# Kernel optimization log

Hardware: AMD Instinct MI355X
Metric: run time of the kernel (lower is better)

Reference implementation:

```python
import jax, jax.numpy as jnp
import numpy as np

N, F, E, C = 50000, 128, 800000, 10

def setup_inputs() -> dict:
    key = jax.random.key(0)
    ks = jax.random.split(key, 16)
    s = 1.0 / np.sqrt(F)
    def u(k, shape):
        return jax.random.uniform(k, shape, jnp.float32, -s, s)
    inp = {
        "x": jax.random.normal(ks[0], (N, F), jnp.float32),
        "edge_index": jax.random.randint(ks[1], (2, E), 0, N),
    }
    for i, p in enumerate(["1", "2"]):
        b = 2 + i * 5
        inp["W" + p] = u(ks[b], (F, F))          # EvolveGCNO initial_weight
        inp["wih" + p] = u(ks[b + 1], (3 * F, F))  # GRU input weights (r,z,n)
        inp["whh" + p] = u(ks[b + 2], (3 * F, F))  # GRU hidden weights
        inp["bih" + p] = u(ks[b + 3], (3 * F,))
        inp["bhh" + p] = u(ks[b + 4], (3 * F,))
    inp["lin_w"] = u(ks[12], (C, F))
    inp["lin_b"] = u(ks[13], (C,))
    return inp

def gru_step(x, h, wih, whh, bih, bhh):
    # torch.nn.GRU single step; gate order r, z, n
    gi = x @ wih.T + bih
    gh = h @ whh.T + bhh
    ir, iz, inn = jnp.split(gi, 3, axis=-1)
    hr, hz, hn = jnp.split(gh, 3, axis=-1)
    r = jax.nn.sigmoid(ir + hr)
    z = jax.nn.sigmoid(iz + hz)
    n = jnp.tanh(inn + r * hn)
    return (1.0 - z) * n + z * h

def gcn_conv(W, x, src, dst):
    # GCNConv_Fixed_W: gcn_norm with self-loops, then aggregate (x @ W)
    n = x.shape[0]
    loop = jnp.arange(n)
    s = jnp.concatenate([src, loop])
    d = jnp.concatenate([dst, loop])
    deg = jax.ops.segment_sum(jnp.ones(s.shape[0], x.dtype), d, num_segments=n)
    dinv = jnp.where(deg > 0, jax.lax.rsqrt(deg), 0.0)
    norm = dinv[s] * dinv[d]                 # [E+N]
    xw = x @ W                               # [N, F]
    return jax.ops.segment_sum(norm[:, None] * xw[s], d, num_segments=n)

def evolve_gcno(x, src, dst, W0, wih, whh, bih, bhh):
    # weight evolved by GRU with input = hidden = current weight
    W = gru_step(W0, W0, wih, whh, bih, bhh)
    return gcn_conv(W, x, src, dst)

def reference(x, edge_index, W1, wih1, whh1, bih1, bhh1,
              W2, wih2, whh2, bih2, bhh2, lin_w, lin_b):
    src, dst = edge_index[0], edge_index[1]
    h = jax.nn.relu(evolve_gcno(x, src, dst, W1, wih1, whh1, bih1, bhh1))
    # dropout is identity in eval mode
    h = jax.nn.relu(evolve_gcno(h, src, dst, W2, wih2, whh2, bih2, bhh2))
    logits = h @ lin_w.T + lin_b
    return jax.nn.log_softmax(logits, axis=1)
```

## Files before the change

kernel.cpp:

```cpp
#include <hip/hip_runtime.h>
#include <cstddef>
#include <cstdint>

#define F 128
#define C_OUT 10
#define SB 256
#define SLOTS 128

typedef short bf16x8 __attribute__((ext_vector_type(8)));
typedef float f32x4  __attribute__((ext_vector_type(4)));
typedef float f32x2  __attribute__((ext_vector_type(2)));

__device__ __forceinline__ unsigned short bf16_rne(float f) {
  unsigned u = __float_as_uint(f);
  return (unsigned short)((u + 0x7FFFu + ((u >> 16) & 1u)) >> 16);
}

__device__ __forceinline__ void gather8(
    const char* p0, const char* p1, const char* p2, const char* p3,
    const char* p4, const char* p5, const char* p6, const char* p7,
    unsigned& u0, unsigned& u1, unsigned& u2, unsigned& u3,
    unsigned& u4, unsigned& u5, unsigned& u6, unsigned& u7) {
  asm volatile(
      "global_load_dword %0, %[q0], off\n\t"
      "global_load_dword %1, %[q1], off\n\t"
      "global_load_dword %2, %[q2], off\n\t"
      "global_load_dword %3, %[q3], off\n\t"
      "global_load_dword %4, %[q4], off\n\t"
      "global_load_dword %5, %[q5], off\n\t"
      "global_load_dword %6, %[q6], off\n\t"
      "global_load_dword %7, %[q7], off\n\t"
      "s_waitcnt vmcnt(0)"
      : "=&v"(u0), "=&v"(u1), "=&v"(u2), "=&v"(u3),
        "=&v"(u4), "=&v"(u5), "=&v"(u6), "=&v"(u7)
      : [q0] "v"(p0), [q1] "v"(p1), [q2] "v"(p2), [q3] "v"(p3),
        [q4] "v"(p4), [q5] "v"(p5), [q6] "v"(p6), [q7] "v"(p7));
}

__device__ __forceinline__ void gather4(
    const char* p0, const char* p1, const char* p2, const char* p3,
    unsigned& u0, unsigned& u1, unsigned& u2, unsigned& u3) {
  asm volatile(
      "global_load_dword %0, %[q0], off\n\t"
      "global_load_dword %1, %[q1], off\n\t"
      "global_load_dword %2, %[q2], off\n\t"
      "global_load_dword %3, %[q3], off\n\t"
      "s_waitcnt vmcnt(0)"
      : "=&v"(u0), "=&v"(u1), "=&v"(u2), "=&v"(u3)
      : [q0] "v"(p0), [q1] "v"(p1), [q2] "v"(p2), [q3] "v"(p3));
}

__global__ void gru_evolve2_k(const float* __restrict__ W01, const float* __restrict__ wih1,
                              const float* __restrict__ whh1, const float* __restrict__ bih1,
                              const float* __restrict__ bhh1,
                              const float* __restrict__ W02, const float* __restrict__ wih2,
                              const float* __restrict__ whh2, const float* __restrict__ bih2,
                              const float* __restrict__ bhh2,
                              unsigned short* __restrict__ Bhi1, unsigned short* __restrict__ Bhi2,
                              int* __restrict__ counts, int n) {
  if ((int)blockIdx.x >= 128) {
    int i = ((int)blockIdx.x - 128) * SB + threadIdx.x;
    if (i < n) counts[i] = 0;
    return;
  }
  int t = blockIdx.x * 256 + threadIdx.x;
  int layer = t >> 14;
  int tt = t & 16383;
  const float* W0  = layer ? W02  : W01;
  const float* wih = layer ? wih2 : wih1;
  const float* whh = layer ? whh2 : whh1;
  const float* bih = layer ? bih2 : bih1;
  const float* bhh = layer ? bhh2 : bhh1;
  unsigned short* Bhi = layer ? Bhi2 : Bhi1;
  int i = tt >> 7, j = tt & 127;
  const float4* w0r = (const float4*)(W0 + (size_t)i * F);
  float gi[3], gh[3];
#pragma unroll
  for (int g = 0; g < 3; ++g) {
    const float4* wr = (const float4*)(wih + (size_t)(g * F + j) * F);
    const float4* hr = (const float4*)(whh + (size_t)(g * F + j) * F);
    float si = 0.f, sh = 0.f;
    for (int k = 0; k < F / 4; ++k) {
      float4 a = w0r[k];
      float4 b = wr[k];
      float4 c = hr[k];
      si += a.x * b.x + a.y * b.y + a.z * b.z + a.w * b.w;
      sh += a.x * c.x + a.y * c.y + a.z * c.z + a.w * c.w;
    }
    gi[g] = si + bih[g * F + j];
    gh[g] = sh + bhh[g * F + j];
  }
  float r = 1.0f / (1.0f + expf(-(gi[0] + gh[0])));
  float z = 1.0f / (1.0f + expf(-(gi[1] + gh[1])));
  float nn = tanhf(gi[2] + r * gh[2]);
  float val = (1.0f - z) * nn + z * W0[(size_t)i * F + j];

  int kstep = i >> 5, kl = i & 31;
  int lane = (kl >> 3) * 16 + (j & 15);
  int tile = j >> 4;
  int idx = ((kstep * 8 + tile) * 64 + lane) * 8 + (kl & 7);
  Bhi[idx] = bf16_rne(val);
}

__global__ void count_rank_k(const int* __restrict__ dst, int* __restrict__ counts,
                             int* __restrict__ rank, int E) {
  int e = blockIdx.x * blockDim.x + threadIdx.x;
  if (e < E) rank[e] = atomicAdd(&counts[dst[e]], 1);
}

__device__ __forceinline__ void fill_body(int bid, const int* __restrict__ src,
                                          const int* __restrict__ dst,
                                          const int* __restrict__ rank,
                                          int* __restrict__ csr_slot, int E) {
  int e = bid * 256 + (int)threadIdx.x;
  if (e < E) {
    int r = rank[e];
    if (r < SLOTS)
      csr_slot[((size_t)dst[e] << 7) + r] = src[e] << 7;
  }
}

__device__ __forceinline__ void gemm_body(int bid, const float* __restrict__ X,
                                          const unsigned short* __restrict__ Bhi,
                                          const int* __restrict__ counts,
                                          unsigned* __restrict__ Y, int nrows) {
  int wid = bid * 4 + ((int)threadIdx.x >> 6);
  int lane = threadIdx.x & 63;
  int ng = (nrows + 15) >> 4;
  if (wid >= ng) return;
  int g = __builtin_amdgcn_readfirstlane(wid);
  int q = lane >> 4, m = lane & 15;
  int rowA = g * 16 + m;
  if (rowA >= nrows) rowA = nrows - 1;

  f32x4 acc[8];
#pragma unroll
  for (int t = 0; t < 8; ++t) { acc[t].x = 0.f; acc[t].y = 0.f; acc[t].z = 0.f; acc[t].w = 0.f; }

#pragma unroll
  for (int s = 0; s < 4; ++s) {
    const float* xp = X + (size_t)rowA * F + s * 32 + q * 8;
    float4 xa = *(const float4*)xp;
    float4 xb = *(const float4*)(xp + 4);
    float xv[8] = {xa.x, xa.y, xa.z, xa.w, xb.x, xb.y, xb.z, xb.w};
    bf16x8 xh;
#pragma unroll
    for (int j = 0; j < 8; ++j) xh[j] = (short)bf16_rne(xv[j]);
#pragma unroll
    for (int t = 0; t < 8; ++t) {
      size_t boff = ((size_t)(s * 8 + t) * 64 + lane) * 8;
      bf16x8 wh = *(const bf16x8*)(Bhi + boff);
      acc[t] = __builtin_amdgcn_mfma_f32_16x16x32_bf16(wh, xh, acc[t], 0, 0, 0);
    }
  }

  int row = g * 16 + m;
  if (row < nrows) {
    float dd = rsqrtf((float)counts[row] + 1.0f);
    unsigned* yr = Y + (size_t)row * 32 + q;
#pragma unroll
    for (int t = 0; t < 8; ++t) {
      int p = __builtin_amdgcn_cvt_pk_fp8_f32(dd * acc[t].x, dd * acc[t].y, 0, false);
      p = __builtin_amdgcn_cvt_pk_fp8_f32(dd * acc[t].z, dd * acc[t].w, p, true);
      yr[t * 4] = (unsigned)p;
    }
  }
}

__global__ void gemm_mfma_k(const float* __restrict__ X, const unsigned short* __restrict__ Bhi,
                            const int* __restrict__ counts, unsigned* __restrict__ Y,
                            int nrows) {
  gemm_body(blockIdx.x, X, Bhi, counts, Y, nrows);
}

__global__ void fill_gemm_k(const float* __restrict__ X, const unsigned short* __restrict__ Bhi,
                            const int* __restrict__ counts, unsigned* __restrict__ Y,
                            int nrows, int ngemm,
                            const int* __restrict__ src, const int* __restrict__ dst,
                            const int* __restrict__ rank, int* __restrict__ csr_slot, int E) {
  if ((int)blockIdx.x < ngemm)
    gemm_body(blockIdx.x, X, Bhi, counts, Y, nrows);
  else
    fill_body((int)blockIdx.x - ngemm, src, dst, rank, csr_slot, E);
}

template <bool FUSE_LOGITS>
__global__ void agg_fp8_k(const int* __restrict__ counts, const int* __restrict__ csr_slot,
                          const unsigned* __restrict__ xwp,
                          float* __restrict__ hout,
                          const float* __restrict__ lw, const float* __restrict__ lb,
                          float* __restrict__ outp, int n) {
  int wave = (int)((blockIdx.x * blockDim.x + threadIdx.x) >> 6);
  int lane = threadIdx.x & 63;
  if (wave >= n) return;
  int node = __builtin_amdgcn_readfirstlane(wave);
  int half = lane >> 5, hm = lane & 31;
  const char* __restrict__ cb = (const char*)xwp;
  unsigned loff = (unsigned)(hm << 2);
  const int* __restrict__ row = csr_slot + ((size_t)node << 7);

  int e = counts[node];
  float dd = rsqrtf((float)e + 1.0f);
  f32x2 acc0 = {0.f, 0.f}, acc1 = {0.f, 0.f};
  f32x2 bcc0 = {0.f, 0.f}, bcc1 = {0.f, 0.f};

#define DEC(U, A, B)                                           \
  do {                                                         \
    (A) += __builtin_amdgcn_cvt_pk_f32_fp8((int)(U), false);   \
    (B) += __builtin_amdgcn_cvt_pk_f32_fp8((int)(U), true);    \
  } while (0)

  {
    unsigned u = *(const unsigned*)(cb + ((((unsigned)node) << 7) | loff));
    if (half) u = 0u;
    DEC(u, acc0, acc1);
  }

  const int* __restrict__ cp = row + half;
  int i = 0;
  for (; i + 16 <= e; i += 16) {
    int s0 = cp[i + 0],  s1 = cp[i + 2],  s2 = cp[i + 4],  s3 = cp[i + 6];
    int s4 = cp[i + 8],  s5 = cp[i + 10], s6 = cp[i + 12], s7 = cp[i + 14];
    unsigned u0, u1, u2, u3, u4, u5, u6, u7;
    gather8(cb + (((unsigned)s0) | loff), cb + (((unsigned)s1) | loff),
            cb + (((unsigned)s2) | loff), cb + (((unsigned)s3) | loff),
            cb + (((unsigned)s4) | loff), cb + (((unsigned)s5) | loff),
            cb + (((unsigned)s6) | loff), cb + (((unsigned)s7) | loff),
            u0, u1, u2, u3, u4, u5, u6, u7);
    DEC(u0, acc0, acc1);
    DEC(u1, bcc0, bcc1);
    DEC(u2, acc0, acc1);
    DEC(u3, bcc0, bcc1);
    DEC(u4, acc0, acc1);
    DEC(u5, bcc0, bcc1);
    DEC(u6, acc0, acc1);
    DEC(u7, bcc0, bcc1);
  }
  if (i + 8 <= e) {
    int s0 = cp[i + 0], s1 = cp[i + 2], s2 = cp[i + 4], s3 = cp[i + 6];
    unsigned u0, u1, u2, u3;
    gather4(cb + (((unsigned)s0) | loff), cb + (((unsigned)s1) | loff),
            cb + (((unsigned)s2) | loff), cb + (((unsigned)s3) | loff),
            u0, u1, u2, u3);
    DEC(u0, acc0, acc1);
    DEC(u1, bcc0, bcc1);
    DEC(u2, acc0, acc1);
    DEC(u3, bcc0, bcc1);
    i += 8;
  }
  if (i + 4 <= e) {
    int s0 = cp[i + 0], s1 = cp[i + 2];
    unsigned u0 = *(const unsigned*)(cb + (((unsigned)s0) | loff));
    unsigned u1 = *(const unsigned*)(cb + (((unsigned)s1) | loff));
    DEC(u0, acc0, acc1);
    DEC(u1, bcc0, bcc1);
    i += 4;
  }
  if (i + 2 <= e) {
    int s0 = cp[i];
    unsigned u = *(const unsigned*)(cb + (((unsigned)s0) | loff));
    DEC(u, acc0, acc1);
    i += 2;
  }
  if (i < e) {
    int idx = i + half;
    if (idx >= e) idx = e - 1;
    int s = row[idx];
    unsigned u = *(const unsigned*)(cb + (((unsigned)s) | loff));
    if (half) u = 0u;
    DEC(u, bcc0, bcc1);
  }
#undef DEC
  acc0 += bcc0;
  acc1 += bcc1;

  acc0.x += __shfl_xor(acc0.x, 32);
  acc0.y += __shfl_xor(acc0.y, 32);
  acc1.x += __shfl_xor(acc1.x, 32);
  acc1.y += __shfl_xor(acc1.y, 32);

  float h0 = fmaxf(dd * acc0.x, 0.f);
  float h1 = fmaxf(dd * acc0.y, 0.f);
  float h2 = fmaxf(dd * acc1.x, 0.f);
  float h3 = fmaxf(dd * acc1.y, 0.f);

  if (!FUSE_LOGITS) {
    if (half == 0) {
      *(float4*)(hout + (size_t)node * F + hm * 4) = make_float4(h0, h1, h2, h3);
    }
  } else {
    float acc[C_OUT];
#pragma unroll
    for (int c = 0; c < C_OUT; ++c) {
      float4 w = *(const float4*)(lw + (size_t)c * F + hm * 4);
      float v = h0 * w.x + h1 * w.y + h2 * w.z + h3 * w.w;
      v += __shfl_xor(v, 1); v += __shfl_xor(v, 2);
      v += __shfl_xor(v, 4); v += __shfl_xor(v, 8);
      v += __shfl_xor(v, 16);
      acc[c] = v + lb[c];
    }
    float mx = acc[0];
#pragma unroll
    for (int c = 1; c < C_OUT; ++c) mx = fmaxf(mx, acc[c]);
    float s = 0.f;
#pragma unroll
    for (int c = 0; c < C_OUT; ++c) s += expf(acc[c] - mx);
    float lse = mx + logf(s);
#pragma unroll
    for (int c = 0; c < C_OUT; ++c)
      if (lane == c) outp[(size_t)node * C_OUT + c] = acc[c] - lse;
  }
}

extern "C" void kernel_launch(void* const* d_in, const int* in_sizes, int n_in,
                              void* d_out, int out_size, void* d_ws, size_t ws_size,
                              hipStream_t stream) {
  const float* x    = (const float*)d_in[0];
  const int*   ei   = (const int*)d_in[1];
  const float* W1   = (const float*)d_in[2];
  const float* wih1 = (const float*)d_in[3];
  const float* whh1 = (const float*)d_in[4];
  const float* bih1 = (const float*)d_in[5];
  const float* bhh1 = (const float*)d_in[6];
  const float* W2   = (const float*)d_in[7];
  const float* wih2 = (const float*)d_in[8];
  const float* whh2 = (const float*)d_in[9];
  const float* bih2 = (const float*)d_in[10];
  const float* bhh2 = (const float*)d_in[11];
  const float* lw   = (const float*)d_in[12];
  const float* lb   = (const float*)d_in[13];
  float* out = (float*)d_out;

  int N = in_sizes[0] / F;
  int E = in_sizes[1] / 2;
  const int* src = ei;
  const int* dst = ei + E;
  int nb = (N + SB - 1) / SB;
  int ng = (N + 15) / 16;
  int ngemm = (ng + 3) / 4;
  int nfill = (E + 255) / 256;
  int nagg = (N + 3) / 4;

  float* ws = (float*)d_ws;
  unsigned* bufA = (unsigned*)ws;
  float* bufB = (float*)(bufA + (size_t)N * 32);
  unsigned short* Bhi1 = (unsigned short*)(bufB + (size_t)N * F);
  unsigned short* Bhi2 = Bhi1 + F * F;
  int* counts = (int*)(Bhi2 + F * F);
  int* rank   = counts + N;
  int* csr_slot = rank + E;

  gru_evolve2_k<<<128 + nb, 256, 0, stream>>>(W1, wih1, whh1, bih1, bhh1,
                                              W2, wih2, whh2, bih2, bhh2,
                                              Bhi1, Bhi2, counts, N);
  count_rank_k<<<(E + 255) / 256, 256, 0, stream>>>(dst, counts, rank, E);
  fill_gemm_k<<<ngemm + nfill, 256, 0, stream>>>(x, Bhi1, counts, bufA, N, ngemm,
                                                 src, dst, rank, csr_slot, E);
  agg_fp8_k<false><<<nagg, 256, 0, stream>>>(counts, csr_slot, bufA, bufB,
                                             nullptr, nullptr, nullptr, N);
  gemm_mfma_k<<<ngemm, 256, 0, stream>>>(bufB, Bhi2, counts, bufA, N);
  agg_fp8_k<true><<<nagg, 256, 0, stream>>>(counts, csr_slot, bufA, nullptr,
                                            lw, lb, out, N);
}
```

Baseline: 258.4 us.

## Fuse all stages into one persistent kernel with grid barriers

Replaces the six-kernel pipeline with a single persistent kernel of 1024 blocks that runs GRU evolution, edge counting and CSR fill, both GEMMs and both aggregations, separated by software grid barriers. The count and fill passes are merged so the rank array is no longer stored, and the layer-1 GEMM main loop runs before the edge pass so its accumulators stay in registers across a barrier. This is meant to remove kernel launch gaps and the rank round-trip through memory. In exchange it depends on all 1024 blocks being co-resident, and it fixes occupancy with launch bounds, uses grid-stride loops for aggregation and adds a memset for the barrier counter.

```diff
diff --git a/kernel.cpp b/kernel.cpp
--- a/kernel.cpp
+++ b/kernel.cpp
@@ -4,8 +4,10 @@
 
 #define F 128
 #define C_OUT 10
-#define SB 256
 #define SLOTS 128
+#define GRID_BLOCKS 1024
+#define NTHR (GRID_BLOCKS * 256)
+#define NWAVES (NTHR / 64)
 
 typedef short bf16x8 __attribute__((ext_vector_type(8)));
 typedef float f32x4  __attribute__((ext_vector_type(4)));
@@ -50,20 +52,26 @@
       : [q0] "v"(p0), [q1] "v"(p1), [q2] "v"(p2), [q3] "v"(p3));
 }
 
-__global__ void gru_evolve2_k(const float* __restrict__ W01, const float* __restrict__ wih1,
-                              const float* __restrict__ whh1, const float* __restrict__ bih1,
-                              const float* __restrict__ bhh1,
-                              const float* __restrict__ W02, const float* __restrict__ wih2,
-                              const float* __restrict__ whh2, const float* __restrict__ bih2,
-                              const float* __restrict__ bhh2,
-                              unsigned short* __restrict__ Bhi1, unsigned short* __restrict__ Bhi2,
-                              int* __restrict__ counts, int n) {
-  if ((int)blockIdx.x >= 128) {
-    int i = ((int)blockIdx.x - 128) * SB + threadIdx.x;
-    if (i < n) counts[i] = 0;
-    return;
-  }
-  int t = blockIdx.x * 256 + threadIdx.x;
+__device__ __forceinline__ void grid_barrier(int* bar, int target) {
+  __syncthreads();
+  if (threadIdx.x == 0) {
+    __threadfence();
+    atomicAdd(bar, 1);
+    while (__hip_atomic_load(bar, __ATOMIC_RELAXED, __HIP_MEMORY_SCOPE_AGENT) < target)
+      __builtin_amdgcn_s_sleep(2);
+    __threadfence();
+  }
+  __syncthreads();
+}
+
+__device__ __forceinline__ void gru_item(int t,
+    const float* __restrict__ W01, const float* __restrict__ wih1,
+    const float* __restrict__ whh1, const float* __restrict__ bih1,
+    const float* __restrict__ bhh1,
+    const float* __restrict__ W02, const float* __restrict__ wih2,
+    const float* __restrict__ whh2, const float* __restrict__ bih2,
+    const float* __restrict__ bhh2,
+    unsigned short* __restrict__ Bhi1, unsigned short* __restrict__ Bhi2) {
   int layer = t >> 14;
   int tt = t & 16383;
   const float* W0  = layer ? W02  : W01;
@@ -102,41 +110,27 @@
   Bhi[idx] = bf16_rne(val);
 }
 
-__global__ void count_rank_k(const int* __restrict__ dst, int* __restrict__ counts,
-                             int* __restrict__ rank, int E) {
-  int e = blockIdx.x * blockDim.x + threadIdx.x;
-  if (e < E) rank[e] = atomicAdd(&counts[dst[e]], 1);
-}
-
-__device__ __forceinline__ void fill_body(int bid, const int* __restrict__ src,
+__device__ __forceinline__ void edge_body(int gt, const int* __restrict__ src,
                                           const int* __restrict__ dst,
-                                          const int* __restrict__ rank,
+                                          int* __restrict__ counts,
                                           int* __restrict__ csr_slot, int E) {
-  int e = bid * 256 + (int)threadIdx.x;
-  if (e < E) {
-    int r = rank[e];
+  for (int e = gt; e < E; e += NTHR) {
+    int d = dst[e];
+    int r = atomicAdd(&counts[d], 1);
     if (r < SLOTS)
-      csr_slot[((size_t)dst[e] << 7) + r] = src[e] << 7;
-  }
-}
-
-__device__ __forceinline__ void gemm_body(int bid, const float* __restrict__ X,
+      csr_slot[((size_t)d << 7) + r] = src[e] << 7;
+  }
+}
+
+__device__ __forceinline__ void gemm_main(int wid, const float* __restrict__ X,
                                           const unsigned short* __restrict__ Bhi,
-                                          const int* __restrict__ counts,
-                                          unsigned* __restrict__ Y, int nrows) {
-  int wid = bid * 4 + ((int)threadIdx.x >> 6);
-  int lane = threadIdx.x & 63;
-  int ng = (nrows + 15) >> 4;
-  if (wid >= ng) return;
+                                          f32x4 acc[8], int nrows, int lane) {
   int g = __builtin_amdgcn_readfirstlane(wid);
   int q = lane >> 4, m = lane & 15;
   int rowA = g * 16 + m;
   if (rowA >= nrows) rowA = nrows - 1;
-
-  f32x4 acc[8];
 #pragma unroll
   for (int t = 0; t < 8; ++t) { acc[t].x = 0.f; acc[t].y = 0.f; acc[t].z = 0.f; acc[t].w = 0.f; }
-
 #pragma unroll
   for (int s = 0; s < 4; ++s) {
     const float* xp = X + (size_t)rowA * F + s * 32 + q * 8;
@@ -153,7 +147,13 @@
       acc[t] = __builtin_amdgcn_mfma_f32_16x16x32_bf16(wh, xh, acc[t], 0, 0, 0);
     }
   }
-
+}
+
+__device__ __forceinline__ void gemm_epi(int wid, const int* __restrict__ counts,
+                                         unsigned* __restrict__ Y, f32x4 acc[8],
+                                         int nrows, int lane) {
+  int g = __builtin_amdgcn_readfirstlane(wid);
+  int q = lane >> 4, m = lane & 15;
   int row = g * 16 + m;
   if (row < nrows) {
     float dd = rsqrtf((float)counts[row] + 1.0f);
@@ -167,33 +167,13 @@
   }
 }
 
-__global__ void gemm_mfma_k(const float* __restrict__ X, const unsigned short* __restrict__ Bhi,
-                            const int* __restrict__ counts, unsigned* __restrict__ Y,
-                            int nrows) {
-  gemm_body(blockIdx.x, X, Bhi, counts, Y, nrows);
-}
-
-__global__ void fill_gemm_k(const float* __restrict__ X, const unsigned short* __restrict__ Bhi,
-                            const int* __restrict__ counts, unsigned* __restrict__ Y,
-                            int nrows, int ngemm,
-                            const int* __restrict__ src, const int* __restrict__ dst,
-                            const int* __restrict__ rank, int* __restrict__ csr_slot, int E) {
-  if ((int)blockIdx.x < ngemm)
-    gemm_body(blockIdx.x, X, Bhi, counts, Y, nrows);
-  else
-    fill_body((int)blockIdx.x - ngemm, src, dst, rank, csr_slot, E);
-}
-
 template <bool FUSE_LOGITS>
-__global__ void agg_fp8_k(const int* __restrict__ counts, const int* __restrict__ csr_slot,
-                          const unsigned* __restrict__ xwp,
-                          float* __restrict__ hout,
-                          const float* __restrict__ lw, const float* __restrict__ lb,
-                          float* __restrict__ outp, int n) {
-  int wave = (int)((blockIdx.x * blockDim.x + threadIdx.x) >> 6);
-  int lane = threadIdx.x & 63;
-  if (wave >= n) return;
-  int node = __builtin_amdgcn_readfirstlane(wave);
+__device__ __forceinline__ void agg_body(int node_in, int lane,
+    const int* __restrict__ counts, const int* __restrict__ csr_slot,
+    const unsigned* __restrict__ xwp, float* __restrict__ hout,
+    const float* __restrict__ lw, const float* __restrict__ lb,
+    float* __restrict__ outp) {
+  int node = __builtin_amdgcn_readfirstlane(node_in);
   int half = lane >> 5, hm = lane & 31;
   const char* __restrict__ cb = (const char*)xwp;
   unsigned loff = (unsigned)(hm << 2);
@@ -312,34 +292,69 @@
   }
 }
 
+struct MegaArgs {
+  const float* x;
+  const int* src;
+  const int* dst;
+  const float *W1, *wih1, *whh1, *bih1, *bhh1;
+  const float *W2, *wih2, *whh2, *bih2, *bhh2;
+  const float *lw, *lb;
+  float* out;
+  unsigned* bufA;
+  float* bufB;
+  unsigned short* Bhi1;
+  unsigned short* Bhi2;
+  int* counts;
+  int* csr_slot;
+  int* bar;
+  int N, E;
+};
+
+__global__ __launch_bounds__(256, 4) void mega_k(MegaArgs a) {
+  int gt = (int)(blockIdx.x * blockDim.x + threadIdx.x);
+  int lane = (int)(threadIdx.x & 63);
+  int wid = gt >> 6;
+  int ng = (a.N + 15) >> 4;
+
+  if (gt < 2 * F * F)
+    gru_item(gt, a.W1, a.wih1, a.whh1, a.bih1, a.bhh1,
+             a.W2, a.wih2, a.whh2, a.bih2, a.bhh2, a.Bhi1, a.Bhi2);
+  for (int i = gt; i < a.N; i += NTHR) a.counts[i] = 0;
+  grid_barrier(a.bar, GRID_BLOCKS * 1);
+
+  f32x4 acc[8];
+  bool hasT = wid < ng;
+  if (hasT) gemm_main(wid, a.x, a.Bhi1, acc, a.N, lane);
+  edge_body(gt, a.src, a.dst, a.counts, a.csr_slot, a.E);
+  grid_barrier(a.bar, GRID_BLOCKS * 2);
+
+  if (hasT) gemm_epi(wid, a.counts, a.bufA, acc, a.N, lane);
+  grid_barrier(a.bar, GRID_BLOCKS * 3);
+
+  for (int node = wid; node < a.N; node += NWAVES)
+    agg_body<false>(node, lane, a.counts, a.csr_slot, a.bufA, a.bufB,
+                    nullptr, nullptr, nullptr);
+  grid_barrier(a.bar, GRID_BLOCKS * 4);
+
+  if (hasT) {
+    gemm_main(wid, a.bufB, a.Bhi2, acc, a.N, lane);
+    gemm_epi(wid, a.counts, a.bufA, acc, a.N, lane);
+  }
+  grid_barrier(a.bar, GRID_BLOCKS * 5);
+
+  for (int node = wid; node < a.N; node += NWAVES)
+    agg_body<true>(node, lane, a.counts, a.csr_slot, a.bufA, nullptr,
+                   a.lw, a.lb, a.out);
+}
+
 extern "C" void kernel_launch(void* const* d_in, const int* in_sizes, int n_in,
                               void* d_out, int out_size, void* d_ws, size_t ws_size,
                               hipStream_t stream) {
   const float* x    = (const float*)d_in[0];
   const int*   ei   = (const int*)d_in[1];
-  const float* W1   = (const float*)d_in[2];
-  const float* wih1 = (const float*)d_in[3];
-  const float* whh1 = (const float*)d_in[4];
-  const float* bih1 = (const float*)d_in[5];
-  const float* bhh1 = (const float*)d_in[6];
-  const float* W2   = (const float*)d_in[7];
-  const float* wih2 = (const float*)d_in[8];
-  const float* whh2 = (const float*)d_in[9];
-  const float* bih2 = (const float*)d_in[10];
-  const float* bhh2 = (const float*)d_in[11];
-  const float* lw   = (const float*)d_in[12];
-  const float* lb   = (const float*)d_in[13];
-  float* out = (float*)d_out;
 
   int N = in_sizes[0] / F;
   int E = in_sizes[1] / 2;
-  const int* src = ei;
-  const int* dst = ei + E;
-  int nb = (N + SB - 1) / SB;
-  int ng = (N + 15) / 16;
-  int ngemm = (ng + 3) / 4;
-  int nfill = (E + 255) / 256;
-  int nagg = (N + 3) / 4;
 
   float* ws = (float*)d_ws;
   unsigned* bufA = (unsigned*)ws;
@@ -347,18 +362,31 @@
   unsigned short* Bhi1 = (unsigned short*)(bufB + (size_t)N * F);
   unsigned short* Bhi2 = Bhi1 + F * F;
   int* counts = (int*)(Bhi2 + F * F);
-  int* rank   = counts + N;
-  int* csr_slot = rank + E;
-
-  gru_evolve2_k<<<128 + nb, 256, 0, stream>>>(W1, wih1, whh1, bih1, bhh1,
-                                              W2, wih2, whh2, bih2, bhh2,
-                                              Bhi1, Bhi2, counts, N);
-  count_rank_k<<<(E + 255) / 256, 256, 0, stream>>>(dst, counts, rank, E);
-  fill_gemm_k<<<ngemm + nfill, 256, 0, stream>>>(x, Bhi1, counts, bufA, N, ngemm,
-                                                 src, dst, rank, csr_slot, E);
-  agg_fp8_k<false><<<nagg, 256, 0, stream>>>(counts, csr_slot, bufA, bufB,
-                                             nullptr, nullptr, nullptr, N);
-  gemm_mfma_k<<<ngemm, 256, 0, stream>>>(bufB, Bhi2, counts, bufA, N);
-  agg_fp8_k<true><<<nagg, 256, 0, stream>>>(counts, csr_slot, bufA, nullptr,
-                                            lw, lb, out, N);
-}
+  int* csr_slot = counts + N;
+  int* bar = csr_slot + (size_t)N * SLOTS;
+
+  MegaArgs a;
+  a.x = x;
+  a.src = ei;
+  a.dst = ei + E;
+  a.W1 = (const float*)d_in[2];  a.wih1 = (const float*)d_in[3];
+  a.whh1 = (const float*)d_in[4]; a.bih1 = (const float*)d_in[5];
+  a.bhh1 = (const float*)d_in[6];
+  a.W2 = (const float*)d_in[7];  a.wih2 = (const float*)d_in[8];
+  a.whh2 = (const float*)d_in[9]; a.bih2 = (const float*)d_in[10];
+  a.bhh2 = (const float*)d_in[11];
+  a.lw = (const float*)d_in[12]; a.lb = (const float*)d_in[13];
+  a.out = (float*)d_out;
+  a.bufA = bufA;
+  a.bufB = bufB;
+  a.Bhi1 = Bhi1;
+  a.Bhi2 = Bhi2;
+  a.counts = counts;
+  a.csr_slot = csr_slot;
+  a.bar = bar;
+  a.N = N;
+  a.E = E;
+
+  hipMemsetAsync(bar, 0, sizeof(int), stream);
+  mega_k<<<GRID_BLOCKS, 256, 0, stream>>>(a);
+}
```

Result: slower. 862.8 us (+233.9%).
